# Kernel tuning notes

Measured on AMD Instinct MI355X. Metric: run time of the kernel, lower is better.

## Reference

```python
import jax, jax.numpy as jnp
import numpy as np

B = 8192          # tokens
H = 7168          # hidden size
E = 256           # routed experts
N_GROUP = 8
GROUP_SIZE = 32   # E // N_GROUP
TOPK_GROUP = 4
TOPK = 8
SCALE = 2.5
EPS = 1e-20
NEG_INF = -jnp.inf


def setup_inputs() -> dict:
    key = jax.random.key(0)
    k1, k2, k3 = jax.random.split(key, 3)
    x = jax.random.normal(k1, (1, 1, B, H), dtype=jnp.float32)
    weight = jax.random.normal(k2, (H, E), dtype=jnp.float32) * 0.02
    bias = jax.random.uniform(k3, (E,), dtype=jnp.float32)  # e_score_correction_bias
    return {"x": x, "weight": weight, "bias": bias}


def reference(x, weight, bias):
    # gate projection + softmax over experts
    logits = jnp.einsum('abth,he->abte', x, weight)          # [1,1,B,E]
    scores = jax.nn.softmax(logits, axis=-1)                 # [1,1,B,E]
    scores_with_bias = scores + bias                         # bias-corrected scores

    # group-limited routing: top-2 per group, summed -> group score
    grouped = scores_with_bias.reshape(1, 1, B, N_GROUP, GROUP_SIZE)
    top2_vals, _ = jax.lax.top_k(grouped, 2)                 # [1,1,B,8,2]
    group_scores = top2_vals.sum(axis=-1)                    # [1,1,B,8]

    # select top-4 groups, build {1, -inf} mask over groups
    _, top4_idx = jax.lax.top_k(group_scores, TOPK_GROUP)    # [1,1,B,4]
    sel = jax.nn.one_hot(top4_idx, N_GROUP, dtype=scores.dtype).sum(axis=-2)  # [1,1,B,8]
    group_mask = jnp.where(sel > 0, 1.0, NEG_INF)
    expert_mask = jnp.repeat(group_mask, GROUP_SIZE, axis=-1)  # [1,1,B,256]

    # mask (multiplicative, as in original), top-8 experts
    masked = scores_with_bias * expert_mask
    _, top8_idx = jax.lax.top_k(masked, TOPK)                # [1,1,B,8]

    # gather unbiased scores, normalize, eps + scale
    w = jnp.take_along_axis(scores, top8_idx, axis=-1)       # [1,1,B,8]
    w = w / w.sum(axis=-1, keepdims=True)
    w = (w + EPS) * SCALE
    return w, top8_idx
```

## Files before the change

kernel.cpp:

```cpp
#include <hip/hip_runtime.h>
#include <math.h>

#define B_TOK 8192
#define H_DIM 7168
#define E_NUM 256
#define NKS   8
#define KSL   (H_DIM / NKS)
#define BK    32
#define NSTEP (KSL / BK)
#define BM    128
#define NMT   (B_TOK / BM)
#define FLAG_CAP 512
#define TAU   2e-6

typedef _Float16 f16;
typedef __attribute__((ext_vector_type(8))) _Float16 f16x8;
typedef __attribute__((ext_vector_type(4))) float    f32x4;

typedef __attribute__((address_space(1))) const void gvoid_t;
typedef __attribute__((address_space(3))) void       lvoid_t;

__device__ inline void gload_lds16(const void* g, void* s) {
    __builtin_amdgcn_global_load_lds((gvoid_t*)g, (lvoid_t*)s, 16, 0, 0);
}

__device__ __forceinline__ void route_token(
    const double* lv, const double* bj, int l, int hf, int t,
    float* __restrict__ out, double* ming_adj, double* ming_grp)
{
    double m = fmax(fmax(lv[0], lv[1]), fmax(lv[2], lv[3]));
    #pragma unroll
    for (int d = 1; d < 64; d <<= 1) m = fmax(m, __shfl_xor(m, d, 64));
    double sc[4], zs = 0.0;
    #pragma unroll
    for (int q = 0; q < 4; ++q) { sc[q] = exp(lv[q] - m); zs += sc[q]; }
    #pragma unroll
    for (int d = 1; d < 64; d <<= 1) zs += __shfl_xor(zs, d, 64);
    double swb[4];
    #pragma unroll
    for (int q = 0; q < 4; ++q) { sc[q] /= zs; swb[q] = sc[q] + bj[q]; }

    double gsq[4];
    #pragma unroll
    for (int q = 0; q < 4; ++q) {
        double a = swb[q], b = -INFINITY;
        #pragma unroll
        for (int d = 1; d <= 16; d <<= 1) {
            double oa = __shfl_xor(a, d, 64), ob = __shfl_xor(b, d, 64);
            double na = fmax(a, oa);
            double nb = fmax(fmin(a, oa), fmax(b, ob));
            a = na; b = nb;
        }
        gsq[q] = a + b;
    }
    double gsv[8];
    #pragma unroll
    for (int q = 0; q < 4; ++q) {
        gsv[2 * q]     = __shfl(gsq[q], 0, 64);
        gsv[2 * q + 1] = __shfl(gsq[q], 32, 64);
    }

    unsigned selmask = 0; double g4 = 0.0, g5 = 0.0;
    #pragma unroll
    for (int k = 0; k < 5; ++k) {
        double best = -INFINITY; int bg = 0;
        #pragma unroll
        for (int g = 0; g < 8; ++g)
            if (gsv[g] > best) { best = gsv[g]; bg = g; }
        if (k < 4) { selmask |= 1u << bg; g4 = best; } else g5 = best;
        #pragma unroll
        for (int g = 0; g < 8; ++g) if (g == bg) gsv[g] = -INFINITY;
    }
    *ming_grp = g4 - g5;

    double mk[4];
    #pragma unroll
    for (int q = 0; q < 4; ++q)
        mk[q] = ((selmask >> (2 * q + hf)) & 1u) ? swb[q] : -INFINITY;

    double wk[8]; int ek[8]; double wsum = 0.0;
    double prev = 0.0, ming = 1e300;
    #pragma unroll
    for (int k = 0; k < 9; ++k) {
        double vbest = mk[0]; int ebest = l;
        #pragma unroll
        for (int q = 1; q < 4; ++q)
            if (mk[q] > vbest) { vbest = mk[q]; ebest = l + 64 * q; }
        #pragma unroll
        for (int d = 1; d < 64; d <<= 1) {
            double ov = __shfl_xor(vbest, d, 64);
            int    oe = __shfl_xor(ebest, d, 64);
            if (ov > vbest || (ov == vbest && oe < ebest)) { vbest = ov; ebest = oe; }
        }
        if (k > 0) ming = fmin(ming, prev - vbest);
        prev = vbest;
        if (k < 8) {
            const int ol = ebest & 63, oq = ebest >> 6;
            if (l == ol) {
                #pragma unroll
                for (int q = 0; q < 4; ++q) if (q == oq) mk[q] = -INFINITY;
            }
            double cand = (oq == 0) ? sc[0] : (oq == 1) ? sc[1] : (oq == 2) ? sc[2] : sc[3];
            double sv = __shfl(cand, ol, 64);
            wk[k] = sv; ek[k] = ebest; wsum += sv;
        }
    }
    *ming_adj = ming;

    if (l == 0) {
        const double inv = 1.0 / wsum;
        #pragma unroll
        for (int k = 0; k < 8; ++k) {
            out[(size_t)t * 8 + k] = (float)((wk[k] * inv + 1e-20) * 2.5);
            out[(size_t)B_TOK * 8 + (size_t)t * 8 + k] = (float)ek[k];
        }
    }
}

__global__ void convert_w_kernel(const float* __restrict__ W,
                                 f16* __restrict__ wpk,
                                 unsigned* __restrict__ flags) {
    if (blockIdx.x == 0 && threadIdx.x == 0) flags[0] = 0;
    int g = blockIdx.x * 256 + threadIdx.x;
    int n = g & 255, k = g >> 8;
    float v = W[(size_t)k * E_NUM + n];
    f16 hi = (f16)v;
    f16 lo = (f16)(v - (float)hi);
    int kf = k >> 5, tq = (k >> 3) & 3, j = k & 7;
    int nf = n >> 4, l = tq * 16 + (n & 15);
    size_t off = ((size_t)(kf * 32 + nf * 2)) * 512 + (size_t)l * 8 + j;
    wpk[off]       = hi;
    wpk[off + 512] = lo;
}

__device__ __forceinline__ void stage_B(const f16* __restrict__ wb, int kf,
                                        char* lds, int wid, int l) {
    #pragma unroll
    for (int i = 0; i < 4; ++i) {
        int fi = wid * 4 + i;
        gload_lds16(wb + ((size_t)kf * 32 + fi) * 512 + (size_t)l * 8,
                    lds + 16384 + fi * 1024);
    }
}

__device__ __forceinline__ void write_A(char* lds, int wid, int l,
                                        float4 a0, float4 a1) {
    float fv[8] = {a0.x, a0.y, a0.z, a0.w, a1.x, a1.y, a1.z, a1.w};
    f16x8 hv, lo;
    #pragma unroll
    for (int j = 0; j < 8; ++j) {
        f16 hh = (f16)fv[j];
        hv[j] = hh;
        lo[j] = (f16)(fv[j] - (float)hh);
    }
    *reinterpret_cast<f16x8*>(&lds[(wid * 2 + 0) * 1024 + l * 16]) = hv;
    *reinterpret_cast<f16x8*>(&lds[(wid * 2 + 1) * 1024 + l * 16]) = lo;
}

__device__ __forceinline__ void compute_step(const char* lds, int wr, int wc,
                                             int l, f32x4 (&acc)[4][4]) {
    const char* Ab = lds;
    const char* Bb = lds + 16384;
    f16x8 af[4][2], bf[4][2];
    #pragma unroll
    for (int mi = 0; mi < 4; ++mi)
        #pragma unroll
        for (int h = 0; h < 2; ++h)
            af[mi][h] = *reinterpret_cast<const f16x8*>(
                Ab + ((wr * 4 + mi) * 2 + h) * 1024 + l * 16);
    #pragma unroll
    for (int ni = 0; ni < 4; ++ni)
        #pragma unroll
        for (int h = 0; h < 2; ++h)
            bf[ni][h] = *reinterpret_cast<const f16x8*>(
                Bb + ((wc * 4 + ni) * 2 + h) * 1024 + l * 16);
    #pragma unroll
    for (int mi = 0; mi < 4; ++mi)
        #pragma unroll
        for (int ni = 0; ni < 4; ++ni) {
            acc[mi][ni] = __builtin_amdgcn_mfma_f32_16x16x32_f16(
                af[mi][0], bf[ni][0], acc[mi][ni], 0, 0, 0);
            acc[mi][ni] = __builtin_amdgcn_mfma_f32_16x16x32_f16(
                af[mi][0], bf[ni][1], acc[mi][ni], 0, 0, 0);
            acc[mi][ni] = __builtin_amdgcn_mfma_f32_16x16x32_f16(
                af[mi][1], bf[ni][0], acc[mi][ni], 0, 0, 0);
        }
}

__global__ __launch_bounds__(512, 4)
void gemm_kernel(const float* __restrict__ x,
                 const f16* __restrict__ wpk,
                 float* __restrict__ partial) {
    __shared__ __align__(16) char lds[49152];

    const int tid = threadIdx.x;
    const int l   = tid & 63;
    const int wid = tid >> 6;
    const int bid = blockIdx.x;
    const int ks  = bid & 7;
    const int mt  = bid >> 3;
    const int wr  = wid >> 2;
    const int wc  = wid & 3;

    const int row = mt * BM + wid * 16 + (l & 15);
    const float* xrow = x + (size_t)row * H_DIM + ks * KSL + (l >> 4) * 8;
    const f16* wb = wpk + (size_t)ks * NSTEP * 32 * 512;

    f32x4 acc[4][4];
    #pragma unroll
    for (int mi = 0; mi < 4; ++mi)
        #pragma unroll
        for (int ni = 0; ni < 4; ++ni) acc[mi][ni] = (f32x4)0.0f;

    float4 a0 = *reinterpret_cast<const float4*>(xrow);
    float4 a1 = *reinterpret_cast<const float4*>(xrow + 4);
    stage_B(wb, 0, lds, wid, l);
    write_A(lds, wid, l, a0, a1);
    a0 = *reinterpret_cast<const float4*>(xrow + BK);
    a1 = *reinterpret_cast<const float4*>(xrow + BK + 4);
    __syncthreads();

    for (int t = 0; t < NSTEP; ++t) {
        float4 a0n, a1n;
        if (t + 2 < NSTEP) {
            a0n = *reinterpret_cast<const float4*>(xrow + (size_t)(t + 2) * BK);
            a1n = *reinterpret_cast<const float4*>(xrow + (size_t)(t + 2) * BK + 4);
        }
        compute_step(lds, wr, wc, l, acc);
        __syncthreads();
        if (t + 1 < NSTEP) {
            stage_B(wb, t + 1, lds, wid, l);
            write_A(lds, wid, l, a0, a1);
            a0 = a0n; a1 = a1n;
            __syncthreads();
        }
    }

    float* pbase = partial + ((size_t)ks * B_TOK + (size_t)mt * BM) * E_NUM;
    #pragma unroll
    for (int mi = 0; mi < 4; ++mi)
        #pragma unroll
        for (int ni = 0; ni < 4; ++ni)
            #pragma unroll
            for (int r = 0; r < 4; ++r) {
                int rr = wr * 64 + mi * 16 + (l >> 4) * 4 + r;
                int cc = wc * 64 + ni * 16 + (l & 15);
                pbase[(size_t)rr * E_NUM + cc] = acc[mi][ni][r];
            }
}

__global__ __launch_bounds__(512, 1)
void routing_kernel(const float* __restrict__ partial,
                    const float* __restrict__ bias,
                    float* __restrict__ out,
                    unsigned* __restrict__ flags) {
    const int tid  = threadIdx.x;
    const int l    = tid & 63;
    const int wv   = tid >> 6;
    const int tok0 = blockIdx.x * 32;

    double bj[4];
    #pragma unroll
    for (int q = 0; q < 4; ++q) bj[q] = (double)bias[l + 64 * q];
    const int hf = l >> 5;

    for (int i = 0; i < 4; ++i) {
        const int t = tok0 + wv * 4 + i;
        double lv[4];
        #pragma unroll
        for (int q = 0; q < 4; ++q) {
            double s = 0.0;
            #pragma unroll
            for (int ksl = 0; ksl < NKS; ++ksl)
                s += (double)partial[((size_t)ksl * B_TOK + t) * E_NUM + l + 64 * q];
            lv[q] = s;
        }
        double ma, mg;
        route_token(lv, bj, l, hf, t, out, &ma, &mg);
        if (l == 0 && (ma < TAU || mg < TAU)) {
            unsigned idx = atomicAdd(&flags[0], 1u);
            if (idx < FLAG_CAP) flags[1 + idx] = (unsigned)t;
        }
    }
}

__global__ __launch_bounds__(256)
void recompute_dot_kernel(const float* __restrict__ x,
                          const float* __restrict__ W,
                          const unsigned* __restrict__ flags,
                          double* __restrict__ dpart) {
    __shared__ float xs[896];
    unsigned count = flags[0]; if (count > FLAG_CAP) count = FLAG_CAP;
    unsigned nj = count * 8;
    for (unsigned j = blockIdx.x; j < nj; j += gridDim.x) {
        unsigned li = j >> 3, sl = j & 7;
        int t = (int)flags[1 + li];
        const float* xb = x + (size_t)t * H_DIM + sl * 896;
        for (int i = threadIdx.x; i < 224; i += 256)
            *reinterpret_cast<float4*>(&xs[i * 4]) =
                *reinterpret_cast<const float4*>(xb + i * 4);
        __syncthreads();
        const float* wp = W + (size_t)(sl * 896) * E_NUM + threadIdx.x;
        double acc = 0.0;
        #pragma unroll 8
        for (int k = 0; k < 896; ++k)
            acc += (double)xs[k] * (double)wp[(size_t)k * E_NUM];
        dpart[((size_t)li * 8 + sl) * E_NUM + threadIdx.x] = acc;
        __syncthreads();
    }
}

__global__ __launch_bounds__(64)
void recompute_route_kernel(const double* __restrict__ dpart,
                            const float* __restrict__ bias,
                            const unsigned* __restrict__ flags,
                            float* __restrict__ out) {
    const int l = threadIdx.x;
    unsigned count = flags[0]; if (count > FLAG_CAP) count = FLAG_CAP;
    double bj[4];
    #pragma unroll
    for (int q = 0; q < 4; ++q) bj[q] = (double)bias[l + 64 * q];
    const int hf = l >> 5;
    for (unsigned li = blockIdx.x; li < count; li += gridDim.x) {
        int t = (int)flags[1 + li];
        double lv[4];
        #pragma unroll
        for (int q = 0; q < 4; ++q) {
            double s = 0.0;
            #pragma unroll
            for (int sl = 0; sl < 8; ++sl)
                s += dpart[((size_t)li * 8 + sl) * E_NUM + l + 64 * q];
            lv[q] = s;
        }
        double ma, mg;
        route_token(lv, bj, l, hf, t, out, &ma, &mg);
    }
}

#define TM 32
#define HB 64
#define FNST (H_DIM / HB)

__global__ __launch_bounds__(512, 1)
void moe_gate_fallback(const float* __restrict__ x,
                       const float* __restrict__ W,
                       const float* __restrict__ bias,
                       float* __restrict__ out) {
    __shared__ double xs[TM][HB];
    const int tid  = threadIdx.x;
    const int l    = tid & 63;
    const int wv   = tid >> 6;
    const int tok0 = blockIdx.x * TM;
    const int tl = tid >> 4;
    const int ho = (tid & 15) * 4;

    double acc[4][4];
    #pragma unroll
    for (int i = 0; i < 4; ++i)
        #pragma unroll
        for (int q = 0; q < 4; ++q) acc[i][q] = 0.0;

    const float* xrow = x + (size_t)(tok0 + tl) * H_DIM + ho;
    float4 v = *reinterpret_cast<const float4*>(xrow);

    for (int s = 0; s < FNST; ++s) {
        __syncthreads();
        xs[tl][ho + 0] = (double)v.x;
        xs[tl][ho + 1] = (double)v.y;
        xs[tl][ho + 2] = (double)v.z;
        xs[tl][ho + 3] = (double)v.w;
        __syncthreads();
        const int sn = (s + 1 < FNST) ? s + 1 : s;
        v = *reinterpret_cast<const float4*>(xrow + (size_t)sn * HB);
        const float* wh = W + (size_t)s * HB * E_NUM + l;
        #pragma unroll 4
        for (int h = 0; h < HB; h += 2) {
            float wf0[4], wf1[4];
            #pragma unroll
            for (int q = 0; q < 4; ++q) {
                wf0[q] = wh[(size_t)h       * E_NUM + q * 64];
                wf1[q] = wh[(size_t)(h + 1) * E_NUM + q * 64];
            }
            #pragma unroll
            for (int i = 0; i < 4; ++i) {
                const double2 xv = *reinterpret_cast<const double2*>(&xs[wv * 4 + i][h]);
                #pragma unroll
                for (int q = 0; q < 4; ++q) {
                    acc[i][q] = fma((double)wf0[q], xv.x, acc[i][q]);
                    acc[i][q] = fma((double)wf1[q], xv.y, acc[i][q]);
                }
            }
        }
    }

    double bj[4];
    #pragma unroll
    for (int q = 0; q < 4; ++q) bj[q] = (double)bias[l + 64 * q];
    const int hf = l >> 5;

    for (int i = 0; i < 4; ++i) {
        const int t = tok0 + wv * 4 + i;
        double lv[4];
        #pragma unroll
        for (int q = 0; q < 4; ++q) lv[q] = acc[i][q];
        double ma, mg;
        route_token(lv, bj, l, hf, t, out, &ma, &mg);
    }
}

extern "C" void kernel_launch(void* const* d_in, const int* in_sizes, int n_in,
                              void* d_out, int out_size, void* d_ws, size_t ws_size,
                              hipStream_t stream) {
    const float* x    = (const float*)d_in[0];
    const float* W    = (const float*)d_in[1];
    const float* bias = (const float*)d_in[2];
    float* out = (float*)d_out;

    const size_t flag_off = 7864320;
    const size_t part_off = 8u * 1024 * 1024;
    const size_t need     = part_off + (size_t)NKS * B_TOK * E_NUM * 4;

    if (ws_size >= need) {
        f16*      wpk     = (f16*)d_ws;
        unsigned* flags   = (unsigned*)((char*)d_ws + flag_off);
        float*    partial = (float*)((char*)d_ws + part_off);
        double*   dpart   = (double*)((char*)d_ws + part_off);

        convert_w_kernel<<<(H_DIM * E_NUM) / 256, 256, 0, stream>>>(W, wpk, flags);
        gemm_kernel<<<NMT * NKS, 512, 0, stream>>>(x, wpk, partial);
        routing_kernel<<<B_TOK / 32, 512, 0, stream>>>(partial, bias, out, flags);
        recompute_dot_kernel<<<1024, 256, 0, stream>>>(x, W, flags, dpart);
        recompute_route_kernel<<<64, 64, 0, stream>>>(dpart, bias, flags, out);
    } else {
        moe_gate_fallback<<<B_TOK / 32, 512, 0, stream>>>(x, W, bias, out);
    }
}
```

Measured before the change: 236.6 us.

## Load A fragments directly to registers and double-buffer B in LDS

The GEMM no longer stages the split-fp16 activation tile through LDS. Each wave now loads and converts its own four A fragments straight into registers, which costs redundant global loads of x across the four column waves. B is double-buffered in two LDS buffers, cutting the barriers per step from two to one so staging overlaps MFMA. The weight conversion kernel is also reworked so each thread writes vectorised 16-byte packed fragments instead of scattered 2-byte stores.

```diff
diff --git a/kernel.cpp b/kernel.cpp
--- a/kernel.cpp
+++ b/kernel.cpp
@@ -121,69 +121,78 @@
                                  f16* __restrict__ wpk,
                                  unsigned* __restrict__ flags) {
     if (blockIdx.x == 0 && threadIdx.x == 0) flags[0] = 0;
-    int g = blockIdx.x * 256 + threadIdx.x;
-    int n = g & 255, k = g >> 8;
-    float v = W[(size_t)k * E_NUM + n];
-    f16 hi = (f16)v;
-    f16 lo = (f16)(v - (float)hi);
-    int kf = k >> 5, tq = (k >> 3) & 3, j = k & 7;
-    int nf = n >> 4, l = tq * 16 + (n & 15);
-    size_t off = ((size_t)(kf * 32 + nf * 2)) * 512 + (size_t)l * 8 + j;
-    wpk[off]       = hi;
-    wpk[off + 512] = lo;
+    int gid = blockIdx.x * 256 + threadIdx.x;
+    int fgp = gid >> 6;
+    int l   = gid & 63;
+    int kf = fgp >> 4, nf = fgp & 15;
+    int rb  = kf * 32 + (l >> 4) * 8;
+    int col = nf * 16 + (l & 15);
+    f16x8 hv, lv;
+    #pragma unroll
+    for (int j = 0; j < 8; ++j) {
+        float v = W[(size_t)(rb + j) * E_NUM + col];
+        f16 hh = (f16)v;
+        hv[j] = hh;
+        lv[j] = (f16)(v - (float)hh);
+    }
+    *reinterpret_cast<f16x8*>(&wpk[(size_t)fgp * 1024 + l * 8])       = hv;
+    *reinterpret_cast<f16x8*>(&wpk[(size_t)fgp * 1024 + 512 + l * 8]) = lv;
 }
 
 __device__ __forceinline__ void stage_B(const f16* __restrict__ wb, int kf,
-                                        char* lds, int wid, int l) {
+                                        char* bbuf, int wid, int l) {
     #pragma unroll
     for (int i = 0; i < 4; ++i) {
         int fi = wid * 4 + i;
         gload_lds16(wb + ((size_t)kf * 32 + fi) * 512 + (size_t)l * 8,
-                    lds + 16384 + fi * 1024);
-    }
-}
-
-__device__ __forceinline__ void write_A(char* lds, int wid, int l,
-                                        float4 a0, float4 a1) {
-    float fv[8] = {a0.x, a0.y, a0.z, a0.w, a1.x, a1.y, a1.z, a1.w};
-    f16x8 hv, lo;
-    #pragma unroll
-    for (int j = 0; j < 8; ++j) {
-        f16 hh = (f16)fv[j];
-        hv[j] = hh;
-        lo[j] = (f16)(fv[j] - (float)hh);
-    }
-    *reinterpret_cast<f16x8*>(&lds[(wid * 2 + 0) * 1024 + l * 16]) = hv;
-    *reinterpret_cast<f16x8*>(&lds[(wid * 2 + 1) * 1024 + l * 16]) = lo;
-}
-
-__device__ __forceinline__ void compute_step(const char* lds, int wr, int wc,
-                                             int l, f32x4 (&acc)[4][4]) {
-    const char* Ab = lds;
-    const char* Bb = lds + 16384;
-    f16x8 af[4][2], bf[4][2];
-    #pragma unroll
-    for (int mi = 0; mi < 4; ++mi)
+                    bbuf + fi * 1024);
+    }
+}
+
+__device__ __forceinline__ void loadA4(const float* const (&xb)[4], int t,
+                                       float4 (&raw)[4][2]) {
+    #pragma unroll
+    for (int mf = 0; mf < 4; ++mf) {
+        raw[mf][0] = *reinterpret_cast<const float4*>(xb[mf] + (size_t)t * BK);
+        raw[mf][1] = *reinterpret_cast<const float4*>(xb[mf] + (size_t)t * BK + 4);
+    }
+}
+
+__device__ __forceinline__ void conv4(const float4 (&raw)[4][2],
+                                      f16x8 (&ah)[4], f16x8 (&al)[4]) {
+    #pragma unroll
+    for (int mf = 0; mf < 4; ++mf) {
+        float fv[8] = {raw[mf][0].x, raw[mf][0].y, raw[mf][0].z, raw[mf][0].w,
+                       raw[mf][1].x, raw[mf][1].y, raw[mf][1].z, raw[mf][1].w};
+        #pragma unroll
+        for (int j = 0; j < 8; ++j) {
+            f16 hh = (f16)fv[j];
+            ah[mf][j] = hh;
+            al[mf][j] = (f16)(fv[j] - (float)hh);
+        }
+    }
+}
+
+__device__ __forceinline__ void mfma_step(const char* bbuf, int wc, int l,
+                                          const f16x8 (&ah)[4], const f16x8 (&al)[4],
+                                          f32x4 (&acc)[4][4]) {
+    f16x8 b[4][2];
+    #pragma unroll
+    for (int ni = 0; ni < 4; ++ni)
         #pragma unroll
         for (int h = 0; h < 2; ++h)
-            af[mi][h] = *reinterpret_cast<const f16x8*>(
-                Ab + ((wr * 4 + mi) * 2 + h) * 1024 + l * 16);
-    #pragma unroll
-    for (int ni = 0; ni < 4; ++ni)
-        #pragma unroll
-        for (int h = 0; h < 2; ++h)
-            bf[ni][h] = *reinterpret_cast<const f16x8*>(
-                Bb + ((wc * 4 + ni) * 2 + h) * 1024 + l * 16);
+            b[ni][h] = *reinterpret_cast<const f16x8*>(
+                bbuf + ((wc * 4 + ni) * 2 + h) * 1024 + l * 16);
     #pragma unroll
     for (int mi = 0; mi < 4; ++mi)
         #pragma unroll
         for (int ni = 0; ni < 4; ++ni) {
             acc[mi][ni] = __builtin_amdgcn_mfma_f32_16x16x32_f16(
-                af[mi][0], bf[ni][0], acc[mi][ni], 0, 0, 0);
+                ah[mi], b[ni][0], acc[mi][ni], 0, 0, 0);
             acc[mi][ni] = __builtin_amdgcn_mfma_f32_16x16x32_f16(
-                af[mi][0], bf[ni][1], acc[mi][ni], 0, 0, 0);
+                ah[mi], b[ni][1], acc[mi][ni], 0, 0, 0);
             acc[mi][ni] = __builtin_amdgcn_mfma_f32_16x16x32_f16(
-                af[mi][1], bf[ni][0], acc[mi][ni], 0, 0, 0);
+                al[mi], b[ni][0], acc[mi][ni], 0, 0, 0);
         }
 }
 
@@ -191,7 +200,8 @@
 void gemm_kernel(const float* __restrict__ x,
                  const f16* __restrict__ wpk,
                  float* __restrict__ partial) {
-    __shared__ __align__(16) char lds[49152];
+    __shared__ __align__(16) char lds0[32768];
+    __shared__ __align__(16) char lds1[32768];
 
     const int tid = threadIdx.x;
     const int l   = tid & 63;
@@ -202,8 +212,12 @@
     const int wr  = wid >> 2;
     const int wc  = wid & 3;
 
-    const int row = mt * BM + wid * 16 + (l & 15);
-    const float* xrow = x + (size_t)row * H_DIM + ks * KSL + (l >> 4) * 8;
+    const float* xb[4];
+    #pragma unroll
+    for (int mf = 0; mf < 4; ++mf) {
+        int row = mt * BM + wr * 64 + mf * 16 + (l & 15);
+        xb[mf] = x + (size_t)row * H_DIM + ks * KSL + (l >> 4) * 8;
+    }
     const f16* wb = wpk + (size_t)ks * NSTEP * 32 * 512;
 
     f32x4 acc[4][4];
@@ -212,28 +226,29 @@
         #pragma unroll
         for (int ni = 0; ni < 4; ++ni) acc[mi][ni] = (f32x4)0.0f;
 
-    float4 a0 = *reinterpret_cast<const float4*>(xrow);
-    float4 a1 = *reinterpret_cast<const float4*>(xrow + 4);
-    stage_B(wb, 0, lds, wid, l);
-    write_A(lds, wid, l, a0, a1);
-    a0 = *reinterpret_cast<const float4*>(xrow + BK);
-    a1 = *reinterpret_cast<const float4*>(xrow + BK + 4);
+    float4 raw[4][2];
+    f16x8  ah[4], al[4];
+
+    stage_B(wb, 0, lds0, wid, l);
+    loadA4(xb, 0, raw);
     __syncthreads();
 
-    for (int t = 0; t < NSTEP; ++t) {
-        float4 a0n, a1n;
+    for (int t = 0; t < NSTEP; t += 2) {
+        stage_B(wb, t + 1, lds1, wid, l);
+        conv4(raw, ah, al);
+        loadA4(xb, t + 1, raw);
+        mfma_step(lds0, wc, l, ah, al, acc);
+        __syncthreads();
+
         if (t + 2 < NSTEP) {
-            a0n = *reinterpret_cast<const float4*>(xrow + (size_t)(t + 2) * BK);
-            a1n = *reinterpret_cast<const float4*>(xrow + (size_t)(t + 2) * BK + 4);
-        }
-        compute_step(lds, wr, wc, l, acc);
-        __syncthreads();
-        if (t + 1 < NSTEP) {
-            stage_B(wb, t + 1, lds, wid, l);
-            write_A(lds, wid, l, a0, a1);
-            a0 = a0n; a1 = a1n;
-            __syncthreads();
-        }
+            stage_B(wb, t + 2, lds0, wid, l);
+            conv4(raw, ah, al);
+            loadA4(xb, t + 2, raw);
+        } else {
+            conv4(raw, ah, al);
+        }
+        mfma_step(lds1, wc, l, ah, al, acc);
+        __syncthreads();
     }
 
     float* pbase = partial + ((size_t)ks * B_TOK + (size_t)mt * BM) * E_NUM;
@@ -426,7 +441,7 @@
         float*    partial = (float*)((char*)d_ws + part_off);
         double*   dpart   = (double*)((char*)d_ws + part_off);
 
-        convert_w_kernel<<<(H_DIM * E_NUM) / 256, 256, 0, stream>>>(W, wpk, flags);
+        convert_w_kernel<<<896, 256, 0, stream>>>(W, wpk, flags);
         gemm_kernel<<<NMT * NKS, 512, 0, stream>>>(x, wpk, partial);
         routing_kernel<<<B_TOK / 32, 512, 0, stream>>>(partial, bias, out, flags);
         recompute_dot_kernel<<<1024, 256, 0, stream>>>(x, W, flags, dpart);
```

After: 721.0 us. 205% more time.
